# Kernel optimization log

Hardware: AMD Instinct MI355X
Metric: run time of the kernel (lower is better)

The kernel has to match this reference:

```python
import jax, jax.numpy as jnp
import numpy as np
from jax import lax

# Dims: B=batch, Cin=in_channel, Ch=channel (bottleneck), Br=breadth (num expert kernels)
B, Cin, Ch, Br, H, W = 16, 256, 128, 8, 64, 64


def setup_inputs() -> dict:
    key = jax.random.key(0)
    ks = jax.random.split(key, 6)
    sc = lambda k, shape: jax.random.normal(k, shape, jnp.float32) * 0.05
    return {
        "x": jax.random.normal(ks[0], (B, Cin, H, W), jnp.float32),
        # SwitchedConv #1: 3x3, in_channel -> channel, breadth expert kernels
        "W1": sc(ks[1], (Br, Ch, Cin, 3, 3)),
        "b1": jnp.zeros((Ch,), jnp.float32),
        # lambda coupler #1: 1x1 projection in_channel -> breadth (per-pixel routing)
        "Wc1": sc(ks[2], (Br, Cin)),
        "bc1": jnp.zeros((Br,), jnp.float32),
        # SwitchedConv #2: 1x1, channel -> in_channel
        "W2": sc(ks[3], (Br, Cin, Ch, 1, 1)),
        "b2": jnp.zeros((Cin,), jnp.float32),
        # lambda coupler #2: 1x1 projection channel -> breadth
        "Wc2": sc(ks[4], (Br, Ch)),
        "bc2": jnp.zeros((Br,), jnp.float32),
    }


def _switched_conv(x, Wk, b, Wc, bc, pad):
    """Input-conditioned mixture of `breadth` conv kernels.

    The coupler (1x1 projection of x to breadth logits, softmax over breadth)
    produces per-pixel mixture weights; each expert kernel's conv output is
    combined per-pixel with these weights.
    x: [B, Cin, H, W]; Wk: [Br, Cout, Cin, k, k]
    """
    br, cout, cin, k, _ = Wk.shape
    bsz, _, h, w = x.shape
    # per-pixel routing weights over the breadth dim: [B, Br, H, W]
    sel = jax.nn.softmax(jnp.einsum('bihw,gi->bghw', x, Wc) + bc[None, :, None, None], axis=1)
    # all breadth branches in one grouped-output conv: [B, Br*Cout, H, W]
    y = lax.conv_general_dilated(
        x, Wk.reshape(br * cout, cin, k, k),
        window_strides=(1, 1), padding=[(pad, pad), (pad, pad)],
        dimension_numbers=('NCHW', 'OIHW', 'NCHW'))
    y = y.reshape(bsz, br, cout, h, w)
    # selection-weighted reduction over breadth + bias
    return jnp.einsum('bgchw,bghw->bchw', y, sel) + b[None, :, None, None]


def reference(x, W1, b1, Wc1, bc1, W2, b2, Wc2, bc2):
    h = jax.nn.relu(x)
    h = _switched_conv(h, W1, b1, Wc1, bc1, pad=1)  # 3x3 switched conv
    h = jax.nn.relu(h)
    h = _switched_conv(h, W2, b2, Wc2, bc2, pad=0)  # 1x1 switched conv
    return h + x  # residual add
```

## Files before the change

kernel.cpp:

```cpp
#include <hip/hip_runtime.h>
#include <hip/hip_bf16.h>
#include <cstdint>

typedef _Float16 h8 __attribute__((ext_vector_type(8)));
typedef _Float16 h4 __attribute__((ext_vector_type(4)));
typedef float    f4 __attribute__((ext_vector_type(4)));
typedef float    fx16 __attribute__((ext_vector_type(16)));


#define GLD16(src, dst) __builtin_amdgcn_global_load_lds( \
    (const __attribute__((address_space(1))) void*)(src), \
    (__attribute__((address_space(3))) void*)(dst), 16, 0, 0)

__global__ __launch_bounds__(256) void prep_w_k(const float* __restrict__ W1,
        const float* __restrict__ W2, _Float16* __restrict__ W1r,
        _Float16* __restrict__ W2r) {
    int i = blockIdx.x * 256 + threadIdx.x;
    if (i < 2359296) {
        int g = i / 294912;  int r  = i - g * 294912;
        int c = r / 2304;    int r2 = r - c * 2304;
        int ci = r2 / 9;     int tap = r2 - ci * 9;
        int s = (ci & 31) >> 3;
        int pos = (s ^ ((c >> 1) & 3)) * 8 + (ci & 7);
        W1r[(((size_t)(ci >> 5) * 9 + tap) * 32768)
            + g * 4096 + c * 32 + pos] = (_Float16)W1[i];
    } else {
        int i2 = i - 2359296;
        int g = i2 >> 15; int r = i2 & 32767; int co = r >> 7; int ch = r & 127;
        W2r[(((size_t)g * 4 + (ch >> 5)) * 256 + co) * 32 + (ch & 31)]
            = (_Float16)W2[i2];
    }
}

__global__ __launch_bounds__(256) void prep_x_k(const float* __restrict__ x,
        const float* __restrict__ Wc1, const float* __restrict__ bc1,
        float* __restrict__ sel1) {
    __shared__ float wc[2048];
    int t = threadIdx.x;
    for (int i = t; i < 2048; i += 256) wc[i] = Wc1[i];
    __syncthreads();
    int pix = blockIdx.x * 256 + t;
    int b = pix >> 12, p = pix & 4095;
    const float* xp = x + (size_t)b * 1048576 + p;
    float lg[8] = {0.f,0.f,0.f,0.f,0.f,0.f,0.f,0.f};
    for (int c = 0; c < 256; ++c) {
        float v = fmaxf(xp[(size_t)c * 4096], 0.f);
        #pragma unroll
        for (int g = 0; g < 8; ++g) lg[g] += wc[g * 256 + c] * v;
    }
    float m = -1e30f;
    #pragma unroll
    for (int g = 0; g < 8; ++g) { lg[g] += bc1[g]; m = fmaxf(m, lg[g]); }
    float sum = 0.f;
    #pragma unroll
    for (int g = 0; g < 8; ++g) { lg[g] = __expf(lg[g] - m); sum += lg[g]; }
    float inv = 1.f / sum;
    #pragma unroll
    for (int g = 0; g < 8; ++g)
        sel1[(size_t)(b * 8 + g) * 4096 + p] = lg[g] * inv;
}

__global__ __launch_bounds__(512, 2) void conv1_k(const float* __restrict__ x,
        const _Float16* __restrict__ W1r, const float* __restrict__ sel1,
        const float* __restrict__ b1, _Float16* __restrict__ hr) {
    __shared__ _Float16 wt[2][32768];
    __shared__ _Float16 xs[12320];
    int t = threadIdx.x;
    int b = blockIdx.y, yt = blockIdx.x;
    int y0 = yt * 4;
    int w = t >> 6, l = t & 63;
    int wm = w >> 1, wn = w & 1;
    int l31 = l & 31, kq2 = l >> 5;
    if (t < 32) xs[12288 + t] = (_Float16)0.f;

    fx16 acc[4];
    #pragma unroll
    for (int n = 0; n < 4; ++n)
        #pragma unroll
        for (int e = 0; e < 16; ++e) acc[n][e] = 0.f;

    {
        const _Float16* srcw = W1r + (size_t)t * 8;
        _Float16* dw = wt[0] + t * 8;
        #pragma unroll
        for (int it = 0; it < 8; ++it)
            GLD16(srcw + it * 4096, dw + it * 4096);
    }

    int px[4];
    #pragma unroll
    for (int nf = 0; nf < 4; ++nf) px[nf] = wn * 128 + nf * 32 + l31;
    bool e0 = (l31 == 0), e63 = (l31 == 31);
    int c = wm * 32 + l31;
    int afo = c * 32 + ((kq2 ^ ((c >> 1) & 3)) * 8);
    int ba[4][3];
    #pragma unroll
    for (int nf = 0; nf < 4; ++nf)
        #pragma unroll
        for (int kx = 0; kx < 3; ++kx) {
            int rz = px[nf] + kx - 1;
            ba[nf][kx] = rz * 32 + ((kq2 ^ ((rz >> 1) & 3)) * 8);
        }
    h8 selv[4];
    #pragma unroll
    for (int nf = 0; nf < 4; ++nf)
        #pragma unroll
        for (int g = 0; g < 8; ++g)
            selv[nf][g] = (_Float16)sel1[(size_t)(b * 8 + g) * 4096 + yt * 256 + px[nf]];

    #pragma unroll 1
    for (int ci = 0; ci < 8; ++ci) {
        __syncthreads();
        if (t < 384) {
            int r = t >> 6, col = t & 63;
            int rc = r * 64 + col;
            int yi = y0 - 1 + r;
            _Float16* dx = xs + rc * 32;
            int rx = (rc >> 1) & 3;
            if (yi >= 0 && yi < 64) {
                const float* xp = x + ((size_t)(b * 256 + ci * 32)) * 4096 + yi * 64 + col;
                float v[32];
                #pragma unroll
                for (int c2 = 0; c2 < 32; ++c2)
                    v[c2] = fmaxf(xp[(size_t)c2 * 4096], 0.f);
                #pragma unroll
                for (int qq = 0; qq < 4; ++qq) {
                    h8 hv;
                    #pragma unroll
                    for (int e = 0; e < 8; ++e) hv[e] = (_Float16)v[qq * 8 + e];
                    *(h8*)(dx + (qq ^ rx) * 8) = hv;
                }
            } else {
                const h8 HZ = {};
                #pragma unroll
                for (int qq = 0; qq < 4; ++qq)
                    *(h8*)(dx + (qq ^ rx) * 8) = HZ;
            }
        }
        #pragma unroll 1
        for (int ky = 0; ky < 3; ++ky) {
            #pragma unroll
            for (int kx = 0; kx < 3; ++kx) {
                int grp = ci * 9 + ky * 3 + kx;
                __syncthreads();
                if (grp < 71) {
                    const _Float16* srcw = W1r + (size_t)(grp + 1) * 32768 + t * 8;
                    _Float16* dw = wt[(grp + 1) & 1] + t * 8;
                    #pragma unroll
                    for (int it = 0; it < 8; ++it)
                        GLD16(srcw + it * 4096, dw + it * 4096);
                }
                const _Float16* wp = wt[grp & 1];
                int ab[4];
                #pragma unroll
                for (int nf = 0; nf < 4; ++nf) {
                    int a = ba[nf][kx] + ky * 2048;
                    if (kx == 0 && !(nf & 1)) a = e0 ? 12288 : a;
                    if (kx == 2 &&  (nf & 1)) a = e63 ? 12288 : a;
                    ab[nf] = a;
                }
                #pragma unroll
                for (int kc = 0; kc < 2; ++kc) {
                    int kco = kc * 16;
                    h8 bfr[4];
                    #pragma unroll
                    for (int nf = 0; nf < 4; ++nf)
                        bfr[nf] = *(const h8*)(xs + (ab[nf] ^ kco));
                    #pragma unroll
                    for (int g = 0; g < 8; ++g) {
                        h8 af = *(const h8*)(wp + g * 4096 + (afo ^ kco));
                        #pragma unroll
                        for (int nf = 0; nf < 4; ++nf) {
                            h8 bs = bfr[nf] * selv[nf][g];
                            acc[nf] = __builtin_amdgcn_mfma_f32_32x32x16_f16(
                                af, bs, acc[nf], 0, 0, 0);
                        }
                    }
                }
            }
        }
    }
    #pragma unroll
    for (int nf = 0; nf < 4; ++nf) {
        size_t pg = ((size_t)(b * 4096 + yt * 256 + px[nf])) * 128;
        #pragma unroll
        for (int q = 0; q < 4; ++q) {
            int c0 = wm * 32 + q * 8 + kq2 * 4;
            f4 bb = *(const f4*)(b1 + c0);
            h4 hv;
            #pragma unroll
            for (int r = 0; r < 4; ++r)
                hv[r] = (_Float16)fmaxf(acc[nf][q * 4 + r] + bb[r], 0.f);
            *(h4*)(hr + pg + c0) = hv;
        }
    }
}

__global__ __launch_bounds__(256) void sel2_k(const _Float16* __restrict__ hr,
        const float* __restrict__ Wc2, const float* __restrict__ bc2,
        float* __restrict__ sel2) {
    __shared__ float wc[1024];
    int t = threadIdx.x;
    for (int i = t; i < 1024; i += 256) wc[i] = Wc2[i];
    __syncthreads();
    int pix = blockIdx.x * 256 + t;
    const h8* hp = (const h8*)(hr + (size_t)pix * 128);
    float lg[8] = {0.f,0.f,0.f,0.f,0.f,0.f,0.f,0.f};
    for (int j = 0; j < 16; ++j) {
        h8 v = hp[j];
        #pragma unroll
        for (int e = 0; e < 8; ++e) {
            float f = (float)v[e];
            int c = j * 8 + e;
            #pragma unroll
            for (int g = 0; g < 8; ++g) lg[g] += wc[g * 128 + c] * f;
        }
    }
    float m = -1e30f;
    #pragma unroll
    for (int g = 0; g < 8; ++g) { lg[g] += bc2[g]; m = fmaxf(m, lg[g]); }
    float sum = 0.f;
    #pragma unroll
    for (int g = 0; g < 8; ++g) { lg[g] = __expf(lg[g] - m); sum += lg[g]; }
    float inv = 1.f / sum;
    int b = pix >> 12, p = pix & 4095;
    #pragma unroll
    for (int g = 0; g < 8; ++g)
        sel2[(size_t)(b * 8 + g) * 4096 + p] = lg[g] * inv;
}

__global__ __launch_bounds__(256, 2) void conv2_k(const _Float16* __restrict__ hr,
        const _Float16* __restrict__ W2r, const float* __restrict__ sel2,
        const float* __restrict__ b2, const float* __restrict__ x,
        float* __restrict__ out) {
    __shared__ _Float16 hs[64 * 128];
    __shared__ _Float16 wt[2][256 * 32];
    int t = threadIdx.x;
    int bid = blockIdx.x;
    int b = bid >> 6, p0 = (bid & 63) * 64;
    int l = t & 63, w = t >> 6;
    int wm = w >> 1, wn = w & 1;
    int l15 = l & 15, sl = l >> 4;
    int swl = (l15 & 7) << 3;
    const f4 FZ = {0.f, 0.f, 0.f, 0.f};
    f4 acce[8][2], accf[8][2];
    #pragma unroll
    for (int m = 0; m < 8; ++m)
        #pragma unroll
        for (int n = 0; n < 2; ++n) { acce[m][n] = FZ; accf[m][n] = FZ; }
    {
        int px = t >> 2, qq = t & 3;
        const _Float16* src = hr + (size_t)(b * 4096 + p0 + px) * 128 + qq * 32;
        #pragma unroll
        for (int u = 0; u < 4; ++u)
            *(h8*)(hs + ((px * 128 + qq * 32 + u * 8) ^ ((px & 7) << 3)))
                = *(const h8*)(src + u * 8);
    }
    float selr[8][2];
    #pragma unroll
    for (int g = 0; g < 8; ++g)
        #pragma unroll
        for (int n = 0; n < 2; ++n)
            selr[g][n] = sel2[(size_t)(b * 8 + g) * 4096 + p0 + wn * 32 + n * 16 + l15];
    int afo[8];
    #pragma unroll
    for (int m = 0; m < 8; ++m) {
        int c = wm * 128 + m * 16 + l15;
        afo[m] = ((c * 32 + sl * 8) ^ swl);
    }
    h8 wr[4];
    auto load_w = [&](int T) {
        const _Float16* srcw = W2r + (size_t)T * 8192;
        #pragma unroll
        for (int it = 0; it < 4; ++it)
            wr[it] = *(const h8*)(srcw + (size_t)(it * 256 + t) * 8);
    };
    auto write_w = [&](int bf) {
        #pragma unroll
        for (int it = 0; it < 4; ++it) {
            int cc = it * 256 + t;
            int c = cc >> 2, q = cc & 3;
            *(h8*)(wt[bf] + ((c * 32 + q * 8) ^ ((c & 7) << 3))) = wr[it];
        }
    };
    load_w(0);
    write_w(0);
    int buf = 0;
    #pragma unroll 1
    for (int T = 0; T < 32; ++T) {
        bool hn = (T < 31);
        if (hn) load_w(T + 1);
        __syncthreads();
        int kc = (T & 3) * 32;
        h8 bfv[2];
        #pragma unroll
        for (int n = 0; n < 2; ++n) {
            int px = wn * 32 + n * 16 + l15;
            bfv[n] = *(const h8*)(hs + ((px * 128 + kc + sl * 8) ^ ((px & 7) << 3)));
        }
        #pragma unroll
        for (int m = 0; m < 8; ++m) {
            h8 af = *(const h8*)(wt[buf] + afo[m]);
            #pragma unroll
            for (int n = 0; n < 2; ++n)
                acce[m][n] = __builtin_amdgcn_mfma_f32_16x16x32_f16(
                    af, bfv[n], acce[m][n], 0, 0, 0);
        }
        if ((T & 3) == 3) {
            int g = T >> 2;
            #pragma unroll
            for (int n = 0; n < 2; ++n)
                #pragma unroll
                for (int m = 0; m < 8; ++m) {
                    accf[m][n] += selr[g][n] * acce[m][n];
                    acce[m][n] = FZ;
                }
        }
        if (hn) write_w(buf ^ 1);
        buf ^= 1;
    }
    #pragma unroll
    for (int m = 0; m < 8; ++m) {
        int c0 = wm * 128 + m * 16 + sl * 4;
        f4 bb = *(const f4*)(b2 + c0);
        #pragma unroll
        for (int n = 0; n < 2; ++n) {
            int px = wn * 32 + n * 16 + l15;
            size_t o = (size_t)(b * 256 + c0) * 4096 + p0 + px;
            #pragma unroll
            for (int r = 0; r < 4; ++r)
                out[o + (size_t)r * 4096] = accf[m][n][r] + bb[r] + x[o + (size_t)r * 4096];
        }
    }
}

extern "C" void kernel_launch(void* const* d_in, const int* in_sizes, int n_in,
                              void* d_out, int out_size, void* d_ws, size_t ws_size,
                              hipStream_t stream) {
    const float* x   = (const float*)d_in[0];
    const float* W1  = (const float*)d_in[1];
    const float* b1  = (const float*)d_in[2];
    const float* Wc1 = (const float*)d_in[3];
    const float* bc1 = (const float*)d_in[4];
    const float* W2  = (const float*)d_in[5];
    const float* b2  = (const float*)d_in[6];
    const float* Wc2 = (const float*)d_in[7];
    const float* bc2 = (const float*)d_in[8];
    float* out = (float*)d_out;
    char* ws = (char*)d_ws;
    _Float16* hr  = (_Float16*)(ws);
    _Float16* W1r = (_Float16*)(ws + 16777216);
    _Float16* W2r = (_Float16*)(ws + 21495808);
    float* sel1   = (float*)(ws + 22020096);
    float* sel2   = (float*)(ws + 24117248);

    hipLaunchKernelGGL(prep_w_k, dim3(10240), dim3(256), 0, stream, W1, W2, W1r, W2r);
    hipLaunchKernelGGL(prep_x_k, dim3(256), dim3(256), 0, stream, x, Wc1, bc1, sel1);
    hipLaunchKernelGGL(conv1_k, dim3(16, 16), dim3(512), 0, stream, x, W1r, sel1, b1, hr);
    hipLaunchKernelGGL(sel2_k, dim3(256), dim3(256), 0, stream, hr, Wc2, bc2, sel2);
    hipLaunchKernelGGL(conv2_k, dim3(1024), dim3(256), 0, stream, hr, W2r, sel2, b2, x, out);
}
```

Measured before the change: 376.0 us.

## Halve conv1 block to 4 waves, each computing two 32-channel M tiles

conv1 now runs with 256 threads instead of 512, and each wave owns 64 output channels (two 32x32 MFMA M-fragments) instead of 32. Each activation fragment, scaled by the routing weight, is then loaded and multiplied once and reused across both weight fragments. This cuts LDS reads and selection multiplies per MFMA. Weight and input-row staging loops are widened so the smaller block still fills the same tiles. The cost is half as many waves per CU to hide latency, plus doubled accumulator register pressure; an unused helper lambda is left in.

```diff
diff --git a/kernel.cpp b/kernel.cpp
--- a/kernel.cpp
+++ b/kernel.cpp
@@ -60,7 +60,7 @@
         sel1[(size_t)(b * 8 + g) * 4096 + p] = lg[g] * inv;
 }
 
-__global__ __launch_bounds__(512, 2) void conv1_k(const float* __restrict__ x,
+__global__ __launch_bounds__(256) void conv1_k(const float* __restrict__ x,
         const _Float16* __restrict__ W1r, const float* __restrict__ sel1,
         const float* __restrict__ b1, _Float16* __restrict__ hr) {
     __shared__ _Float16 wt[2][32768];
@@ -73,26 +73,34 @@
     int l31 = l & 31, kq2 = l >> 5;
     if (t < 32) xs[12288 + t] = (_Float16)0.f;
 
-    fx16 acc[4];
-    #pragma unroll
-    for (int n = 0; n < 4; ++n)
-        #pragma unroll
-        for (int e = 0; e < 16; ++e) acc[n][e] = 0.f;
-
-    {
-        const _Float16* srcw = W1r + (size_t)t * 8;
-        _Float16* dw = wt[0] + t * 8;
-        #pragma unroll
-        for (int it = 0; it < 8; ++it)
-            GLD16(srcw + it * 4096, dw + it * 4096);
-    }
+    fx16 acc[2][4];
+    #pragma unroll
+    for (int m = 0; m < 2; ++m)
+        #pragma unroll
+        for (int n = 0; n < 4; ++n)
+            #pragma unroll
+            for (int e = 0; e < 16; ++e) acc[m][n][e] = 0.f;
+
+    auto stage_w = [&](int T, _Float16* dwb) {
+        const _Float16* srcw = W1r + (size_t)T * 32768 + t * 8;
+        _Float16* dw = dwb + t * 8;
+        #pragma unroll
+        for (int it = 0; it < 16; ++it)
+            GLD16(srcw + it * 2048, dw + it * 2048);
+    };
 
     int px[4];
     #pragma unroll
     for (int nf = 0; nf < 4; ++nf) px[nf] = wn * 128 + nf * 32 + l31;
     bool e0 = (l31 == 0), e63 = (l31 == 31);
-    int c = wm * 32 + l31;
-    int afo = c * 32 + ((kq2 ^ ((c >> 1) & 3)) * 8);
+    int afo[2][2];
+    #pragma unroll
+    for (int m = 0; m < 2; ++m)
+        #pragma unroll
+        for (int kc = 0; kc < 2; ++kc) {
+            int c = wm * 64 + m * 32 + l31;
+            afo[m][kc] = c * 32 + (((kc * 2 + kq2) ^ ((c >> 1) & 3)) * 8);
+        }
     int ba[4][3];
     #pragma unroll
     for (int nf = 0; nf < 4; ++nf)
@@ -108,72 +116,125 @@
         for (int g = 0; g < 8; ++g)
             selv[nf][g] = (_Float16)sel1[(size_t)(b * 8 + g) * 4096 + yt * 256 + px[nf]];
 
+    auto stage_row = [&](int r) {
+        int col = t & 63;
+        int rc = r * 64 + col;
+        int yi = y0 - 1 + r;
+        _Float16* dx = xs + rc * 32;
+        int rx = (rc >> 1) & 3;
+        if (yi >= 0 && yi < 64) {
+            const float* xp2 = x + ((size_t)(b * 256)) * 4096 + yi * 64 + col;
+            float v[32];
+            #pragma unroll
+            for (int c2 = 0; c2 < 32; ++c2)
+                v[c2] = fmaxf(xp2[(size_t)c2 * 4096], 0.f);
+            #pragma unroll
+            for (int qq = 0; qq < 4; ++qq) {
+                h8 hv;
+                #pragma unroll
+                for (int e = 0; e < 8; ++e) hv[e] = (_Float16)v[qq * 8 + e];
+                *(h8*)(dx + (qq ^ rx) * 8) = hv;
+            }
+        } else {
+            const h8 HZ = {};
+            #pragma unroll
+            for (int qq = 0; qq < 4; ++qq)
+                *(h8*)(dx + (qq ^ rx) * 8) = HZ;
+        }
+    };
+
+    stage_w(0, wt[0]);
     #pragma unroll 1
     for (int ci = 0; ci < 8; ++ci) {
         __syncthreads();
-        if (t < 384) {
-            int r = t >> 6, col = t & 63;
-            int rc = r * 64 + col;
-            int yi = y0 - 1 + r;
-            _Float16* dx = xs + rc * 32;
-            int rx = (rc >> 1) & 3;
-            if (yi >= 0 && yi < 64) {
-                const float* xp = x + ((size_t)(b * 256 + ci * 32)) * 4096 + yi * 64 + col;
-                float v[32];
-                #pragma unroll
-                for (int c2 = 0; c2 < 32; ++c2)
-                    v[c2] = fmaxf(xp[(size_t)c2 * 4096], 0.f);
-                #pragma unroll
-                for (int qq = 0; qq < 4; ++qq) {
-                    h8 hv;
-                    #pragma unroll
-                    for (int e = 0; e < 8; ++e) hv[e] = (_Float16)v[qq * 8 + e];
-                    *(h8*)(dx + (qq ^ rx) * 8) = hv;
+        {
+            const float* xci = x + (size_t)ci * 32 * 4096;
+            (void)xci;
+            int r = t >> 6;
+            {
+                int col = t & 63;
+                int rc = r * 64 + col;
+                int yi = y0 - 1 + r;
+                _Float16* dx = xs + rc * 32;
+                int rx = (rc >> 1) & 3;
+                if (yi >= 0 && yi < 64) {
+                    const float* xp2 = x + ((size_t)(b * 256 + ci * 32)) * 4096 + yi * 64 + col;
+                    float v[32];
+                    #pragma unroll
+                    for (int c2 = 0; c2 < 32; ++c2)
+                        v[c2] = fmaxf(xp2[(size_t)c2 * 4096], 0.f);
+                    #pragma unroll
+                    for (int qq = 0; qq < 4; ++qq) {
+                        h8 hv;
+                        #pragma unroll
+                        for (int e = 0; e < 8; ++e) hv[e] = (_Float16)v[qq * 8 + e];
+                        *(h8*)(dx + (qq ^ rx) * 8) = hv;
+                    }
+                } else {
+                    const h8 HZ = {};
+                    #pragma unroll
+                    for (int qq = 0; qq < 4; ++qq)
+                        *(h8*)(dx + (qq ^ rx) * 8) = HZ;
                 }
-            } else {
-                const h8 HZ = {};
-                #pragma unroll
-                for (int qq = 0; qq < 4; ++qq)
-                    *(h8*)(dx + (qq ^ rx) * 8) = HZ;
+            }
+            if (t < 128) {
+                int r2 = 4 + (t >> 6);
+                int col = t & 63;
+                int rc = r2 * 64 + col;
+                int yi = y0 - 1 + r2;
+                _Float16* dx = xs + rc * 32;
+                int rx = (rc >> 1) & 3;
+                if (yi >= 0 && yi < 64) {
+                    const float* xp2 = x + ((size_t)(b * 256 + ci * 32)) * 4096 + yi * 64 + col;
+                    float v[32];
+                    #pragma unroll
+                    for (int c2 = 0; c2 < 32; ++c2)
+                        v[c2] = fmaxf(xp2[(size_t)c2 * 4096], 0.f);
+                    #pragma unroll
+                    for (int qq = 0; qq < 4; ++qq) {
+                        h8 hv;
+                        #pragma unroll
+                        for (int e = 0; e < 8; ++e) hv[e] = (_Float16)v[qq * 8 + e];
+                        *(h8*)(dx + (qq ^ rx) * 8) = hv;
+                    }
+                } else {
+                    const h8 HZ = {};
+                    #pragma unroll
+                    for (int qq = 0; qq < 4; ++qq)
+                        *(h8*)(dx + (qq ^ rx) * 8) = HZ;
+                }
             }
         }
         #pragma unroll 1
         for (int ky = 0; ky < 3; ++ky) {
             #pragma unroll
             for (int kx = 0; kx < 3; ++kx) {
-                int grp = ci * 9 + ky * 3 + kx;
+                int T = ci * 9 + ky * 3 + kx;
                 __syncthreads();
-                if (grp < 71) {
-                    const _Float16* srcw = W1r + (size_t)(grp + 1) * 32768 + t * 8;
-                    _Float16* dw = wt[(grp + 1) & 1] + t * 8;
-                    #pragma unroll
-                    for (int it = 0; it < 8; ++it)
-                        GLD16(srcw + it * 4096, dw + it * 4096);
-                }
-                const _Float16* wp = wt[grp & 1];
-                int ab[4];
+                if (T < 71) stage_w(T + 1, wt[(T + 1) & 1]);
+                h8 bfr[4][2];
                 #pragma unroll
                 for (int nf = 0; nf < 4; ++nf) {
                     int a = ba[nf][kx] + ky * 2048;
                     if (kx == 0 && !(nf & 1)) a = e0 ? 12288 : a;
                     if (kx == 2 &&  (nf & 1)) a = e63 ? 12288 : a;
-                    ab[nf] = a;
+                    bfr[nf][0] = *(const h8*)(xs + a);
+                    bfr[nf][1] = *(const h8*)(xs + (a ^ 16));
                 }
+                const _Float16* wp = wt[T & 1];
                 #pragma unroll
-                for (int kc = 0; kc < 2; ++kc) {
-                    int kco = kc * 16;
-                    h8 bfr[4];
-                    #pragma unroll
-                    for (int nf = 0; nf < 4; ++nf)
-                        bfr[nf] = *(const h8*)(xs + (ab[nf] ^ kco));
-                    #pragma unroll
-                    for (int g = 0; g < 8; ++g) {
-                        h8 af = *(const h8*)(wp + g * 4096 + (afo ^ kco));
+                for (int g = 0; g < 8; ++g) {
+                    #pragma unroll
+                    for (int kc = 0; kc < 2; ++kc) {
+                        h8 a0 = *(const h8*)(wp + g * 4096 + afo[0][kc]);
+                        h8 a1 = *(const h8*)(wp + g * 4096 + afo[1][kc]);
                         #pragma unroll
                         for (int nf = 0; nf < 4; ++nf) {
-                            h8 bs = bfr[nf] * selv[nf][g];
-                            acc[nf] = __builtin_amdgcn_mfma_f32_32x32x16_f16(
-                                af, bs, acc[nf], 0, 0, 0);
+                            h8 bs = bfr[nf][kc] * selv[nf][g];
+                            acc[0][nf] = __builtin_amdgcn_mfma_f32_32x32x16_f16(
+                                a0, bs, acc[0][nf], 0, 0, 0);
+                            acc[1][nf] = __builtin_amdgcn_mfma_f32_32x32x16_f16(
+                                a1, bs, acc[1][nf], 0, 0, 0);
                         }
                     }
                 }
@@ -181,19 +242,21 @@
         }
     }
     #pragma unroll
-    for (int nf = 0; nf < 4; ++nf) {
-        size_t pg = ((size_t)(b * 4096 + yt * 256 + px[nf])) * 128;
-        #pragma unroll
-        for (int q = 0; q < 4; ++q) {
-            int c0 = wm * 32 + q * 8 + kq2 * 4;
-            f4 bb = *(const f4*)(b1 + c0);
-            h4 hv;
-            #pragma unroll
-            for (int r = 0; r < 4; ++r)
-                hv[r] = (_Float16)fmaxf(acc[nf][q * 4 + r] + bb[r], 0.f);
-            *(h4*)(hr + pg + c0) = hv;
-        }
-    }
+    for (int m = 0; m < 2; ++m)
+        #pragma unroll
+        for (int nf = 0; nf < 4; ++nf) {
+            size_t pg = ((size_t)(b * 4096 + yt * 256 + px[nf])) * 128;
+            #pragma unroll
+            for (int q = 0; q < 4; ++q) {
+                int c0 = wm * 64 + m * 32 + q * 8 + kq2 * 4;
+                f4 bb = *(const f4*)(b1 + c0);
+                h4 hv;
+                #pragma unroll
+                for (int r = 0; r < 4; ++r)
+                    hv[r] = (_Float16)fmaxf(acc[m][nf][q * 4 + r] + bb[r], 0.f);
+                *(h4*)(hr + pg + c0) = hv;
+            }
+        }
 }
 
 __global__ __launch_bounds__(256) void sel2_k(const _Float16* __restrict__ hr,
@@ -356,7 +419,7 @@
 
     hipLaunchKernelGGL(prep_w_k, dim3(10240), dim3(256), 0, stream, W1, W2, W1r, W2r);
     hipLaunchKernelGGL(prep_x_k, dim3(256), dim3(256), 0, stream, x, Wc1, bc1, sel1);
-    hipLaunchKernelGGL(conv1_k, dim3(16, 16), dim3(512), 0, stream, x, W1r, sel1, b1, hr);
+    hipLaunchKernelGGL(conv1_k, dim3(16, 16), dim3(256), 0, stream, x, W1r, sel1, b1, hr);
     hipLaunchKernelGGL(sel2_k, dim3(256), dim3(256), 0, stream, hr, Wc2, bc2, sel2);
     hipLaunchKernelGGL(conv2_k, dim3(1024), dim3(256), 0, stream, hr, W2r, sel2, b2, x, out);
 }
```

New measurement: 396.9 us. 5.6% more time.
